# Optimization experiments

Hardware: AMD Instinct MI355X
Metric: run time of the kernel (lower is better)

The kernel has to match this reference:

```python
import jax, jax.numpy as jnp
import numpy as np

N, T, D_FEAT, D_GATE, D_MODEL = 1024, 32, 158, 63, 256
T_NHEAD, S_NHEAD, BETA = 4, 2, 5.0


def _pe(seq_len, d_model):
    pos = np.arange(seq_len, dtype=np.float32)[:, None]
    div = np.exp(np.arange(0, d_model, 2, dtype=np.float32) * (-np.log(10000.0) / d_model))
    pe = np.zeros((seq_len, d_model), np.float32)
    pe[:, 0::2] = np.sin(pos * div)
    pe[:, 1::2] = np.cos(pos * div)
    return jnp.asarray(pe)


def _ln(x, g, b):
    m = jnp.mean(x, -1, keepdims=True)
    v = jnp.var(x, -1, keepdims=True)
    return (x - m) / jnp.sqrt(v + 1e-5) * g + b


def _attn_block(x, n1g, n1b, Wq, Wk, Wv, n2g, n2b, W1, b1, W2, b2, nhead, over_stocks):
    # Faithful to SAttention/TAttention: per-head split of equally-sized dims is
    # equivalent to a single batched multi-head attention. Dropout p=0 (eval).
    n, t, d = x.shape
    dh = d // nhead
    temp = float(np.sqrt(d / nhead))
    xn = _ln(x, n1g, n1b)
    q = (xn @ Wq).reshape(n, t, nhead, dh)
    k = (xn @ Wk).reshape(n, t, nhead, dh)
    v = (xn @ Wv).reshape(n, t, nhead, dh)
    if over_stocks:
        # attention across stocks, per time step: scores [T,H,N,N]
        s = jnp.einsum('qthd,kthd->thqk', q, k) / temp
        a = jax.nn.softmax(s, -1)
        o = jnp.einsum('thqk,kthd->qthd', a, v).reshape(n, t, d)
    else:
        # attention across time, per stock: scores [N,H,T,T]
        s = jnp.einsum('nqhd,nkhd->nhqk', q, k) / temp
        a = jax.nn.softmax(s, -1)
        o = jnp.einsum('nhqk,nkhd->nqhd', a, v).reshape(n, t, d)
    xt = _ln(xn + o, n2g, n2b)
    ffn = jnp.maximum(xt @ W1 + b1, 0.0) @ W2 + b2
    return xt + ffn


def _forward(x, gate_W, gate_b, feat_W, feat_b, ds_mid_W, ds_mid_b, ds_small_W, ds_small_b,
             tn1g, tn1b, tWq, tWk, tWv, tn2g, tn2b, tW1, tb1, tW2, tb2,
             sn1g, sn1b, sWq, sWk, sWv, sn2g, sn2b, sW1, sb1, sW2, sb2,
             temp_W, fus_W, fus_b, fus_g, fus_bb, dec_W, dec_b):
    src = x[:, :, :D_FEAT]                       # [N,T,158]
    gate_in = x[:, -1, D_FEAT:]                  # [N,63] market features at last step
    g = D_FEAT * jax.nn.softmax((gate_in @ gate_W + gate_b) / BETA, -1)
    src = src * g[:, None, :]
    h = src @ feat_W + feat_b + _pe(T, D_MODEL)  # [N,32,256]
    # multi-scale downsampling: AvgPool1d k=2/s=2 and k=4/s=4 along time
    h_mid = h.reshape(N, T // 2, 2, D_MODEL).mean(2) @ ds_mid_W + ds_mid_b
    h_small = h.reshape(N, T // 4, 4, D_MODEL).mean(2) @ ds_small_W + ds_small_b
    pooled = []
    for hs in (h, h_mid, h_small):
        z = _attn_block(hs, tn1g, tn1b, tWq, tWk, tWv, tn2g, tn2b, tW1, tb1, tW2, tb2,
                        T_NHEAD, over_stocks=False)
        z = _attn_block(z, sn1g, sn1b, sWq, sWk, sWv, sn2g, sn2b, sW1, sb1, sW2, sb2,
                        S_NHEAD, over_stocks=True)
        # TemporalAttention pooling: query = last-step projection
        hh = z @ temp_W
        lam = jax.nn.softmax(jnp.einsum('ntd,nd->nt', hh, hh[:, -1, :]), -1)
        pooled.append(jnp.einsum('nt,ntd->nd', lam, z))
    fused = jnp.concatenate(pooled, -1) @ fus_W + fus_b
    fused = jnp.maximum(_ln(fused, fus_g, fus_bb), 0.0)
    return (fused @ dec_W + dec_b).squeeze(-1)    # [N]


def setup_inputs() -> dict:
    key = jax.random.key(0)
    ks = iter(jax.random.split(key, 40))
    w = lambda shape: jax.random.normal(next(ks), shape, jnp.float32) * 0.02
    d = D_MODEL
    inp = {
        'x': jax.random.normal(next(ks), (N, T, D_FEAT + D_GATE), jnp.float32),
        'gate_W': w((D_GATE, D_FEAT)), 'gate_b': jnp.zeros((D_FEAT,), jnp.float32),
        'feat_W': w((D_FEAT, d)), 'feat_b': jnp.zeros((d,), jnp.float32),
        'ds_mid_W': w((d, d)), 'ds_mid_b': jnp.zeros((d,), jnp.float32),
        'ds_small_W': w((d, d)), 'ds_small_b': jnp.zeros((d,), jnp.float32),
        'tn1g': jnp.ones((d,), jnp.float32), 'tn1b': jnp.zeros((d,), jnp.float32),
        'tWq': w((d, d)), 'tWk': w((d, d)), 'tWv': w((d, d)),
        'tn2g': jnp.ones((d,), jnp.float32), 'tn2b': jnp.zeros((d,), jnp.float32),
        'tW1': w((d, d)), 'tb1': jnp.zeros((d,), jnp.float32),
        'tW2': w((d, d)), 'tb2': jnp.zeros((d,), jnp.float32),
        'sn1g': jnp.ones((d,), jnp.float32), 'sn1b': jnp.zeros((d,), jnp.float32),
        'sWq': w((d, d)), 'sWk': w((d, d)), 'sWv': w((d, d)),
        'sn2g': jnp.ones((d,), jnp.float32), 'sn2b': jnp.zeros((d,), jnp.float32),
        'sW1': w((d, d)), 'sb1': jnp.zeros((d,), jnp.float32),
        'sW2': w((d, d)), 'sb2': jnp.zeros((d,), jnp.float32),
        'temp_W': w((d, d)),
        'fus_W': w((3 * d, d)), 'fus_b': jnp.zeros((d,), jnp.float32),
        'fus_g': jnp.ones((d,), jnp.float32), 'fus_bb': jnp.zeros((d,), jnp.float32),
        'dec_W': w((d, 1)), 'dec_b': jnp.zeros((1,), jnp.float32),
    }
    return inp


def reference(x, gate_W, gate_b, feat_W, feat_b, ds_mid_W, ds_mid_b, ds_small_W, ds_small_b,
              tn1g, tn1b, tWq, tWk, tWv, tn2g, tn2b, tW1, tb1, tW2, tb2,
              sn1g, sn1b, sWq, sWk, sWv, sn2g, sn2b, sW1, sb1, sW2, sb2,
              temp_W, fus_W, fus_b, fus_g, fus_bb, dec_W, dec_b):
    return _forward(x, gate_W, gate_b, feat_W, feat_b, ds_mid_W, ds_mid_b, ds_small_W, ds_small_b,
                    tn1g, tn1b, tWq, tWk, tWv, tn2g, tn2b, tW1, tb1, tW2, tb2,
                    sn1g, sn1b, sWq, sWk, sWv, sn2g, sn2b, sW1, sb1, sW2, sb2,
                    temp_W, fus_W, fus_b, fus_g, fus_bb, dec_W, dec_b)
```

## Files before the change

kernel.cpp:

```cpp
#include <hip/hip_runtime.h>
#include <math.h>

#define NS 1024
#define T0 32
#define DF 158
#define DG 63
#define DM 256
#define XROW (DF + DG)
#define MTOT 57344
#define B1R 32768
#define B2R 49152

typedef unsigned short u16;
typedef __attribute__((ext_vector_type(8))) short bf16x8_t;
typedef __attribute__((ext_vector_type(4))) float f32x4_t;

union frag_u {
  bf16x8_t f;
  unsigned short us[8];
  unsigned int u32[4];
};

__device__ inline unsigned short f2bf(float x) {
  unsigned int u = __float_as_uint(x);
  unsigned int r = u + 0x7fffu + ((u >> 16) & 1u);
  return (unsigned short)(r >> 16);
}
__device__ inline float bf2f(u16 u) {
  return __uint_as_float(((unsigned int)u) << 16);
}
__device__ inline unsigned int cvtpk(float a, float b) {
  unsigned int r;
  asm("v_cvt_pk_bf16_f32 %0, %1, %2" : "=v"(r) : "v"(a), "v"(b));
  return r;
}
__device__ inline void gl16(const u16* gp, unsigned char* lp) {
  __builtin_amdgcn_global_load_lds((const __attribute__((address_space(1))) unsigned int*)gp,
                                   (__attribute__((address_space(3))) unsigned int*)lp, 16, 0, 0);
}

__global__ void k_pe(float* __restrict__ pe) {
  int t = blockIdx.x, d = threadIdx.x;
  int i2 = d & ~1;
  float div = expf((float)i2 * (-logf(10000.0f) / (float)DM));
  float ang = (float)t * div;
  pe[t * DM + d] = (d & 1) ? cosf(ang) : sinf(ang);
}

__global__ void k_gate(const float* __restrict__ x, const float* __restrict__ gW,
                       const float* __restrict__ gb, float* __restrict__ g) {
  int n = blockIdx.x, tid = threadIdx.x;
  __shared__ float gin[DG];
  __shared__ float red[256];
  if (tid < DG) gin[tid] = x[(size_t)n * T0 * XROW + 31 * XROW + DF + tid];
  __syncthreads();
  float myv = 0.f;
  if (tid < DF) {
    float acc = gb[tid];
    for (int j = 0; j < DG; j++) acc = fmaf(gin[j], gW[j * DF + tid], acc);
    myv = acc * (1.0f / 5.0f);
  }
  red[tid] = (tid < DF) ? myv : -1e30f;
  __syncthreads();
  for (int s = 128; s > 0; s >>= 1) { if (tid < s) red[tid] = fmaxf(red[tid], red[tid + s]); __syncthreads(); }
  float mx = red[0];
  __syncthreads();
  float e = (tid < DF) ? expf(myv - mx) : 0.f;
  red[tid] = e;
  __syncthreads();
  for (int s = 128; s > 0; s >>= 1) { if (tid < s) red[tid] += red[tid + s]; __syncthreads(); }
  float sum = red[0];
  if (tid < DF) g[(size_t)n * DF + tid] = (float)DF * e / sum;
}

struct WPrep { const float* s[14]; float sc[14]; };
__global__ __launch_bounds__(256) void k_wprep(WPrep w, u16* __restrict__ dst) {
  int mat = blockIdx.x >> 4, nb = blockIdx.x & 15;
  int tid = threadIdx.x;
  int n = nb * 16 + (tid >> 4);
  int kc = (tid & 15) * 16;
  const float* src = w.s[mat];
  float sc = w.sc[mat];
  int K = (mat == 0) ? DF : 256;
  frag_u f0, f1;
#pragma unroll
  for (int j = 0; j < 8; j++) {
    int k0 = kc + j, k1 = kc + 8 + j;
    f0.us[j] = (k0 < K) ? f2bf(src[(size_t)k0 * 256 + n] * sc) : (u16)0;
    f1.us[j] = (k1 < K) ? f2bf(src[(size_t)k1 * 256 + n] * sc) : (u16)0;
  }
  u16* d = dst + (size_t)mat * 65536 + (size_t)n * 256 + kc;
  *(bf16x8_t*)d = f0.f;
  *(bf16x8_t*)(d + 8) = f1.f;
}

__global__ __launch_bounds__(256) void k_wtrans(const float* __restrict__ W, u16* __restrict__ Wt) {
  __shared__ u16 Ts[64][65];
  int k0 = blockIdx.x * 64, n0 = blockIdx.y * 64;
  int tid = threadIdx.x;
#pragma unroll
  for (int i = 0; i < 16; i++) {
    int e = tid + i * 256;
    int r = e >> 6, c = e & 63;
    Ts[r][c] = f2bf(W[(size_t)(k0 + r) * 256 + n0 + c]);
  }
  __syncthreads();
#pragma unroll
  for (int i = 0; i < 16; i++) {
    int e = tid + i * 256;
    int r = e >> 6, c = e & 63;
    Wt[(size_t)(n0 + r) * 768 + k0 + c] = Ts[c][r];
  }
}

template <bool BIAS, bool RELU, bool RES, bool OUTBF>
__global__ __launch_bounds__(256) void k_bgemm(
    const u16* __restrict__ A,
    const u16* __restrict__ B0, const u16* __restrict__ B1, const u16* __restrict__ B2,
    const float* __restrict__ bias, const u16* __restrict__ res,
    void* __restrict__ C0, void* __restrict__ C1, void* __restrict__ C2) {
  __shared__ __align__(16) unsigned char sm[32768];
  unsigned char* As = sm;
  unsigned char* Bs = sm + 16384;
  const u16* Bt = blockIdx.z == 0 ? B0 : (blockIdx.z == 1 ? B1 : B2);
  void* Cv = blockIdx.z == 0 ? C0 : (blockIdx.z == 1 ? C1 : C2);
  int m0 = blockIdx.y * 128, n0w = blockIdx.x * 128;
  int tid = threadIdx.x, lane = tid & 63, wid = tid >> 6;
  int qi = lane & 15, g = lane >> 4;
  int wr = wid >> 1, wc = wid & 1;
  f32x4_t acc[4][4];
#pragma unroll
  for (int i = 0; i < 4; i++)
#pragma unroll
    for (int j = 0; j < 4; j++) acc[i][j] = (f32x4_t){0.f, 0.f, 0.f, 0.f};
  for (int kt = 0; kt < 4; kt++) {
    if (kt) __syncthreads();
#pragma unroll
    for (int i = 0; i < 4; i++) {
      int cid = tid + i * 256;
      int row = cid >> 3, c = cid & 7;
      int cs = c ^ (row & 7);
      gl16(A + (size_t)(m0 + row) * 256 + kt * 64 + cs * 8, As + cid * 16);
      gl16(Bt + (size_t)(n0w + row) * 256 + kt * 64 + cs * 8, Bs + cid * 16);
    }
    __syncthreads();
    bf16x8_t Af[2][4], Bf[2][4];
#pragma unroll
    for (int mi = 0; mi < 4; mi++) {
      int row = wr * 64 + mi * 16 + qi;
      int swz = (row & 7) << 4;
      const unsigned char* ap = As + row * 128;
      Af[0][mi] = *(const bf16x8_t*)(ap + ((g * 16) ^ swz));
      Af[1][mi] = *(const bf16x8_t*)(ap + ((64 + g * 16) ^ swz));
    }
#pragma unroll
    for (int ni = 0; ni < 4; ni++) {
      int row = wc * 64 + ni * 16 + qi;
      int swz = (row & 7) << 4;
      const unsigned char* bp = Bs + row * 128;
      Bf[0][ni] = *(const bf16x8_t*)(bp + ((g * 16) ^ swz));
      Bf[1][ni] = *(const bf16x8_t*)(bp + ((64 + g * 16) ^ swz));
    }
#pragma unroll
    for (int ks = 0; ks < 2; ks++)
#pragma unroll
      for (int mi = 0; mi < 4; mi++)
#pragma unroll
        for (int ni = 0; ni < 4; ni++)
          acc[mi][ni] = __builtin_amdgcn_mfma_f32_16x16x32_bf16(Af[ks][mi], Bf[ks][ni], acc[mi][ni], 0, 0, 0);
  }
#pragma unroll
  for (int mi = 0; mi < 4; mi++) {
#pragma unroll
    for (int ni = 0; ni < 4; ni++) {
#pragma unroll
      for (int r = 0; r < 4; r++) {
        int row = m0 + wr * 64 + mi * 16 + 4 * g + r;
        int col = n0w + wc * 64 + ni * 16 + qi;
        float vv = acc[mi][ni][r];
        if (BIAS) vv += bias[col];
        if (RES) vv += bf2f(res[(size_t)row * 256 + col]);
        if (RELU) vv = fmaxf(vv, 0.f);
        if (OUTBF) ((u16*)Cv)[(size_t)row * 256 + col] = f2bf(vv);
        else ((float*)Cv)[(size_t)row * 256 + col] = vv;
      }
    }
  }
}

__global__ __launch_bounds__(256) void k_fgemm(
    const float* __restrict__ x, const float* __restrict__ gate,
    const u16* __restrict__ Bt, const float* __restrict__ bias,
    const float* __restrict__ pe, float* __restrict__ C) {
  __shared__ __align__(16) unsigned char sm[32768];
  unsigned char* As = sm;
  unsigned char* Bs = sm + 16384;
  int m0 = blockIdx.y * 128, n0w = blockIdx.x * 128;
  int tid = threadIdx.x, lane = tid & 63, wid = tid >> 6;
  int qi = lane & 15, g = lane >> 4;
  int wr = wid >> 1, wc = wid & 1;
  f32x4_t acc[4][4];
#pragma unroll
  for (int i = 0; i < 4; i++)
#pragma unroll
    for (int j = 0; j < 4; j++) acc[i][j] = (f32x4_t){0.f, 0.f, 0.f, 0.f};
  for (int kt = 0; kt < 3; kt++) {
    if (kt) __syncthreads();
#pragma unroll
    for (int i = 0; i < 4; i++) {
      int cid = tid + i * 256;
      int row = cid >> 3, c = cid & 7;
      int swz = (c * 16) ^ ((row & 7) << 4);
      int gk0 = kt * 64 + c * 8;
      const float* xr = x + (size_t)(m0 + row) * XROW;
      const float* gr = gate + (size_t)((m0 + row) >> 5) * DF;
      frag_u f;
#pragma unroll
      for (int j = 0; j < 8; j++) {
        int gk = gk0 + j;
        f.us[j] = (gk < DF) ? f2bf(xr[gk] * gr[gk]) : (u16)0;
      }
      *(bf16x8_t*)(As + row * 128 + swz) = f.f;
      bf16x8_t vb = *(const bf16x8_t*)(Bt + (size_t)(n0w + row) * 256 + kt * 64 + c * 8);
      *(bf16x8_t*)(Bs + row * 128 + swz) = vb;
    }
    __syncthreads();
    bf16x8_t Af[2][4], Bf[2][4];
#pragma unroll
    for (int mi = 0; mi < 4; mi++) {
      int row = wr * 64 + mi * 16 + qi;
      int swz = (row & 7) << 4;
      const unsigned char* ap = As + row * 128;
      Af[0][mi] = *(const bf16x8_t*)(ap + ((g * 16) ^ swz));
      Af[1][mi] = *(const bf16x8_t*)(ap + ((64 + g * 16) ^ swz));
    }
#pragma unroll
    for (int ni = 0; ni < 4; ni++) {
      int row = wc * 64 + ni * 16 + qi;
      int swz = (row & 7) << 4;
      const unsigned char* bp = Bs + row * 128;
      Bf[0][ni] = *(const bf16x8_t*)(bp + ((g * 16) ^ swz));
      Bf[1][ni] = *(const bf16x8_t*)(bp + ((64 + g * 16) ^ swz));
    }
#pragma unroll
    for (int ks = 0; ks < 2; ks++)
#pragma unroll
      for (int mi = 0; mi < 4; mi++)
#pragma unroll
        for (int ni = 0; ni < 4; ni++)
          acc[mi][ni] = __builtin_amdgcn_mfma_f32_16x16x32_bf16(Af[ks][mi], Bf[ks][ni], acc[mi][ni], 0, 0, 0);
  }
#pragma unroll
  for (int mi = 0; mi < 4; mi++) {
#pragma unroll
    for (int ni = 0; ni < 4; ni++) {
#pragma unroll
      for (int r = 0; r < 4; r++) {
        int row = m0 + wr * 64 + mi * 16 + 4 * g + r;
        int col = n0w + wc * 64 + ni * 16 + qi;
        C[(size_t)row * 256 + col] = acc[mi][ni][r] + bias[col] + pe[(row & (T0 - 1)) * DM + col];
      }
    }
  }
}

__global__ __launch_bounds__(256) void k_fus(const u16* __restrict__ A, const u16* __restrict__ Bt,
                                             const float* __restrict__ bias, float* __restrict__ C) {
  __shared__ __align__(16) unsigned char sm[16384];
  unsigned char* As = sm;
  unsigned char* Bs = sm + 8192;
  int n0 = blockIdx.x * 64, m0 = blockIdx.y * 64;
  int tid = threadIdx.x, lane = tid & 63, wid = tid >> 6;
  int qi = lane & 15, g = lane >> 4;
  f32x4_t acc[4];
#pragma unroll
  for (int i = 0; i < 4; i++) acc[i] = (f32x4_t){0.f, 0.f, 0.f, 0.f};
  for (int kt = 0; kt < 12; kt++) {
    if (kt) __syncthreads();
#pragma unroll
    for (int i = 0; i < 2; i++) {
      int cid = tid + i * 256;
      int row = cid >> 3, c = cid & 7;
      int swz = (c * 16) ^ ((row & 7) << 4);
      *(bf16x8_t*)(As + row * 128 + swz) = *(const bf16x8_t*)(A + (size_t)(m0 + row) * 768 + kt * 64 + c * 8);
      *(bf16x8_t*)(Bs + row * 128 + swz) = *(const bf16x8_t*)(Bt + (size_t)(n0 + row) * 768 + kt * 64 + c * 8);
    }
    __syncthreads();
    int arow = wid * 16 + qi;
    int asw = (arow & 7) << 4;
    bf16x8_t Af0 = *(const bf16x8_t*)(As + arow * 128 + ((g * 16) ^ asw));
    bf16x8_t Af1 = *(const bf16x8_t*)(As + arow * 128 + ((64 + g * 16) ^ asw));
#pragma unroll
    for (int ni = 0; ni < 4; ni++) {
      int brow = ni * 16 + qi;
      int bsw = (brow & 7) << 4;
      bf16x8_t B0 = *(const bf16x8_t*)(Bs + brow * 128 + ((g * 16) ^ bsw));
      bf16x8_t B1 = *(const bf16x8_t*)(Bs + brow * 128 + ((64 + g * 16) ^ bsw));
      acc[ni] = __builtin_amdgcn_mfma_f32_16x16x32_bf16(Af0, B0, acc[ni], 0, 0, 0);
      acc[ni] = __builtin_amdgcn_mfma_f32_16x16x32_bf16(Af1, B1, acc[ni], 0, 0, 0);
    }
  }
#pragma unroll
  for (int ni = 0; ni < 4; ni++)
#pragma unroll
    for (int r = 0; r < 4; r++) {
      int row = m0 + wid * 16 + 4 * g + r;
      int col = n0 + ni * 16 + qi;
      C[(size_t)row * 256 + col] = acc[ni][r] + bias[col];
    }
}

template <bool RES, bool ABF>
__global__ __launch_bounds__(256) void k_ln(const void* __restrict__ a, const float* __restrict__ b,
                                            const float* __restrict__ g, const float* __restrict__ be,
                                            u16* __restrict__ out) {
  int row = blockIdx.x * 4 + (threadIdx.x >> 6);
  int lane = threadIdx.x & 63;
  size_t base = (size_t)row * DM + lane * 4;
  float v[4];
  if (ABF) {
    ushort4 u = *(const ushort4*)((const u16*)a + base);
    v[0] = bf2f(u.x); v[1] = bf2f(u.y); v[2] = bf2f(u.z); v[3] = bf2f(u.w);
  } else {
    f32x4_t t = *(const f32x4_t*)((const float*)a + base);
    v[0] = t[0]; v[1] = t[1]; v[2] = t[2]; v[3] = t[3];
  }
  if (RES) {
    f32x4_t t = *(const f32x4_t*)(b + base);
    v[0] += t[0]; v[1] += t[1]; v[2] += t[2]; v[3] += t[3];
  }
  float s = v[0] + v[1] + v[2] + v[3];
#pragma unroll
  for (int off = 1; off < 64; off <<= 1) s += __shfl_xor(s, off);
  float mean = s * (1.0f / DM);
  float d0 = v[0] - mean, d1 = v[1] - mean, d2 = v[2] - mean, d3 = v[3] - mean;
  float ss = d0 * d0 + d1 * d1 + d2 * d2 + d3 * d3;
#pragma unroll
  for (int off = 1; off < 64; off <<= 1) ss += __shfl_xor(ss, off);
  float inv = rsqrtf(ss * (1.0f / DM) + 1e-5f);
  f32x4_t gg = *(const f32x4_t*)(g + lane * 4);
  f32x4_t bb = *(const f32x4_t*)(be + lane * 4);
  ushort4 o4;
  o4.x = f2bf(d0 * inv * gg[0] + bb[0]);
  o4.y = f2bf(d1 * inv * gg[1] + bb[1]);
  o4.z = f2bf(d2 * inv * gg[2] + bb[2]);
  o4.w = f2bf(d3 * inv * gg[3] + bb[3]);
  *(ushort4*)(out + base) = o4;
}

__global__ void k_poolmean(const float* __restrict__ h, u16* __restrict__ out, int Tout, int P) {
  int vi = blockIdx.x * 256 + threadIdx.x;
  int dv = vi & 63;
  int rowi = vi >> 6;
  int to = rowi % Tout;
  int n = rowi / Tout;
  int Tin = Tout * P;
  float s0 = 0.f, s1 = 0.f, s2 = 0.f, s3 = 0.f;
  for (int p = 0; p < P; p++) {
    f32x4_t t = *(const f32x4_t*)(h + ((size_t)(n * Tin + to * P + p)) * DM + dv * 4);
    s0 += t[0]; s1 += t[1]; s2 += t[2]; s3 += t[3];
  }
  float inv = 1.0f / (float)P;
  ushort4 o4;
  o4.x = f2bf(s0 * inv); o4.y = f2bf(s1 * inv); o4.z = f2bf(s2 * inv); o4.w = f2bf(s3 * inv);
  *(ushort4*)(out + (size_t)rowi * DM + dv * 4) = o4;
}

template <int T>
__global__ __launch_bounds__(256) void k_tattn(const u16* __restrict__ q, const u16* __restrict__ k,
                                               const u16* __restrict__ v, float* __restrict__ o) {
  constexpr int TR = (T < 16) ? 16 : T;
  constexpr int QKB = TR * 128;
  constexpr int HS = 2 * QKB + 64 * 80;
  __shared__ __align__(16) unsigned char smem[4 * HS];
  int n = blockIdx.x;
  int tid = threadIdx.x, lane = tid & 63, h = tid >> 6;
  int qi = lane & 15, g = lane >> 4;
  unsigned char* Qs = smem + h * HS;
  unsigned char* Ks = Qs + QKB;
  unsigned char* Vt = Ks + QKB;

  const u16* qh = q + (size_t)n * T * 256 + h * 64;
  const u16* kh = k + (size_t)n * T * 256 + h * 64;
  const u16* vh = v + (size_t)n * T * 256 + h * 64;
  const bf16x8_t zero8 = {0, 0, 0, 0, 0, 0, 0, 0};

  for (int idx = lane; idx < TR * 8; idx += 64) {
    int row = idx >> 3, c = idx & 7;
    bf16x8_t vq = zero8, vk = zero8;
    if (row < T) {
      vq = *(const bf16x8_t*)(qh + (size_t)row * 256 + c * 8);
      vk = *(const bf16x8_t*)(kh + (size_t)row * 256 + c * 8);
    }
    int off = row * 128 + ((c * 16) ^ ((row & 7) << 4));
    *(bf16x8_t*)(Qs + off) = vq;
    *(bf16x8_t*)(Ks + off) = vk;
  }
  {
    int kp = lane & 15, dg = lane >> 4;
    int d0 = dg * 16;
    int kk = 2 * kp;
    int cb = ((((kk >> 2) & 3) << 3) | (((kk >> 4) & 1) << 2) | (kk & 3)) * 2;
    frag_u a0, a1, b0, b1;
    a0.f = a1.f = b0.f = b1.f = zero8;
    if (kk < T) {
      a0.f = *(const bf16x8_t*)(vh + (size_t)kk * 256 + d0);
      a1.f = *(const bf16x8_t*)(vh + (size_t)kk * 256 + d0 + 8);
    }
    if (kk + 1 < T) {
      b0.f = *(const bf16x8_t*)(vh + (size_t)(kk + 1) * 256 + d0);
      b1.f = *(const bf16x8_t*)(vh + (size_t)(kk + 1) * 256 + d0 + 8);
    }
#pragma unroll
    for (int i = 0; i < 8; i++)
      *(unsigned int*)(Vt + (d0 + i) * 80 + cb) = (unsigned int)a0.us[i] | ((unsigned int)b0.us[i] << 16);
#pragma unroll
    for (int i = 0; i < 8; i++)
      *(unsigned int*)(Vt + (d0 + 8 + i) * 80 + cb) = (unsigned int)a1.us[i] | ((unsigned int)b1.us[i] << 16);
  }
  __syncthreads();

  constexpr int NQT = (T == 32) ? 2 : 1;
  constexpr int NSUB = (T == 32) ? 2 : 1;

  bf16x8_t Qb[NQT][2];
#pragma unroll
  for (int qt = 0; qt < NQT; qt++) {
    int row = qt * 16 + qi;
    int sw = (row & 7) << 4;
#pragma unroll
    for (int kst = 0; kst < 2; kst++)
      Qb[qt][kst] = *(const bf16x8_t*)(Qs + row * 128 + ((kst * 64 + g * 16) ^ sw));
  }
  f32x4_t sacc[NQT][NSUB];
#pragma unroll
  for (int qt = 0; qt < NQT; qt++)
#pragma unroll
    for (int sub = 0; sub < NSUB; sub++) sacc[qt][sub] = (f32x4_t){0.f, 0.f, 0.f, 0.f};
#pragma unroll
  for (int sub = 0; sub < NSUB; sub++) {
    int row = sub * 16 + qi;
    int sw = (row & 7) << 4;
    bf16x8_t Ka[2];
#pragma unroll
    for (int kst = 0; kst < 2; kst++)
      Ka[kst] = *(const bf16x8_t*)(Ks + row * 128 + ((kst * 64 + g * 16) ^ sw));
#pragma unroll
    for (int qt = 0; qt < NQT; qt++)
#pragma unroll
      for (int kst = 0; kst < 2; kst++)
        sacc[qt][sub] = __builtin_amdgcn_mfma_f32_16x16x32_bf16(Ka[kst], Qb[qt][kst], sacc[qt][sub], 0, 0, 0);
  }
  frag_u Pf[NQT];
#pragma unroll
  for (int qt = 0; qt < NQT; qt++) {
    float sv[NSUB][4];
    float mx = -3.0e38f;
#pragma unroll
    for (int sub = 0; sub < NSUB; sub++)
#pragma unroll
      for (int r = 0; r < 4; r++) {
        int key = sub * 16 + 4 * g + r;
        float s = sacc[qt][sub][r];
        if (key >= T) s = -3.0e38f;
        sv[sub][r] = s;
        mx = fmaxf(mx, s);
      }
    mx = fmaxf(mx, __shfl_xor(mx, 16));
    mx = fmaxf(mx, __shfl_xor(mx, 32));
    float p[NSUB][4];
    float l = 0.f;
#pragma unroll
    for (int sub = 0; sub < NSUB; sub++)
#pragma unroll
      for (int r = 0; r < 4; r++) {
        float e = exp2f(sv[sub][r] - mx);
        p[sub][r] = e;
        l += e;
      }
    l += __shfl_xor(l, 16);
    l += __shfl_xor(l, 32);
    float linv = 1.0f / l;
    Pf[qt].u32[0] = cvtpk(p[0][0] * linv, p[0][1] * linv);
    Pf[qt].u32[1] = cvtpk(p[0][2] * linv, p[0][3] * linv);
    if (NSUB == 2) {
      Pf[qt].u32[2] = cvtpk(p[NSUB - 1][0] * linv, p[NSUB - 1][1] * linv);
      Pf[qt].u32[3] = cvtpk(p[NSUB - 1][2] * linv, p[NSUB - 1][3] * linv);
    } else {
      Pf[qt].u32[2] = 0u;
      Pf[qt].u32[3] = 0u;
    }
  }
  f32x4_t oacc[NQT][4];
#pragma unroll
  for (int qt = 0; qt < NQT; qt++)
#pragma unroll
    for (int ni = 0; ni < 4; ni++) oacc[qt][ni] = (f32x4_t){0.f, 0.f, 0.f, 0.f};
#pragma unroll
  for (int ni = 0; ni < 4; ni++) {
    bf16x8_t Vb = *(const bf16x8_t*)(Vt + (ni * 16 + qi) * 80 + g * 16);
#pragma unroll
    for (int qt = 0; qt < NQT; qt++)
      oacc[qt][ni] = __builtin_amdgcn_mfma_f32_16x16x32_bf16(Pf[qt].f, Vb, oacc[qt][ni], 0, 0, 0);
  }
#pragma unroll
  for (int qt = 0; qt < NQT; qt++)
#pragma unroll
    for (int ni = 0; ni < 4; ni++)
#pragma unroll
      for (int r = 0; r < 4; r++) {
        int qq = qt * 16 + 4 * g + r;
        if (qq < T) o[((size_t)(n * T + qq)) * 256 + h * 64 + ni * 16 + qi] = oacc[qt][ni][r];
      }
}

__global__ __launch_bounds__(256) void k_sattn(const u16* __restrict__ q, const u16* __restrict__ k,
                                               const u16* __restrict__ v, float* __restrict__ o) {
  __shared__ __align__(16) unsigned char smem[32768];
  unsigned char* Ks = smem;
  unsigned char* Vt = smem + 16384;

  int bid = blockIdx.x;
  int T, rowbase;
  if (bid < 512) { T = 32; rowbase = 0; }
  else if (bid < 768) { T = 16; rowbase = B1R; bid -= 512; }
  else { T = 8; rowbase = B2R; bid -= 768; }
  const int NTH = T * 2;
  int xcd = bid & 7, slot = bid >> 3;
  int th = xcd * (NTH >> 3) + (slot >> 3);
  int qb = slot & 7;
  int t = th >> 1, h = th & 1;

  int tid = threadIdx.x;
  int lane = tid & 63;
  int wid = tid >> 6;
  int qi = lane & 15;
  int g = lane >> 4;

  const size_t rs = (size_t)T * 256;
  const size_t hb = (size_t)rowbase * 256 + (size_t)t * 256 + h * 128;
  const u16* qp = q + hb;
  const u16* kp = k + hb;
  const u16* vp = v + hb;
  float* op = o + hb;

  int q0 = qb * 128 + wid * 32;

  bf16x8_t QfA[4], QfB[4];
  {
    const u16* sA = qp + (size_t)(q0 + qi) * rs + g * 8;
    const u16* sB = sA + 16 * rs;
#pragma unroll
    for (int kst = 0; kst < 4; kst++) {
      QfA[kst] = *(const bf16x8_t*)(sA + kst * 32);
      QfB[kst] = *(const bf16x8_t*)(sB + kst * 32);
    }
  }

  f32x4_t OA[8], OB[8];
#pragma unroll
  for (int i = 0; i < 8; i++) {
    OA[i] = (f32x4_t){0.f, 0.f, 0.f, 0.f};
    OB[i] = (f32x4_t){0.f, 0.f, 0.f, 0.f};
  }
  float mA = -3.0e38f, lA = 0.f, mB = -3.0e38f, lB = 0.f;

  int kpair = tid & 31, dg = tid >> 5;
  int d0s = dg * 16;
  int kk = 2 * kpair;
  int cb = (((kk >> 5) << 5) | (((kk >> 2) & 3) << 3) | (((kk >> 4) & 1) << 2) | (kk & 3)) * 2;

  for (int kb = 0; kb < NS; kb += 64) {
    __syncthreads();
#pragma unroll
    for (int i = 0; i < 4; i++) {
      int cid = tid + i * 256;
      int row = cid >> 4, ch = cid & 15;
      bf16x8_t kv = *(const bf16x8_t*)(kp + (size_t)(kb + row) * rs + ch * 8);
      *(bf16x8_t*)(Ks + row * 256 + ((ch * 16) ^ ((row & 7) << 4))) = kv;
    }
    {
      const u16* s0 = vp + (size_t)(kb + kk) * rs + d0s;
      const u16* s1 = s0 + rs;
      frag_u a0, a1, b0, b1;
      a0.f = *(const bf16x8_t*)s0;
      a1.f = *(const bf16x8_t*)(s0 + 8);
      b0.f = *(const bf16x8_t*)s1;
      b1.f = *(const bf16x8_t*)(s1 + 8);
#pragma unroll
      for (int i = 0; i < 8; i++) {
        int d = d0s + i;
        *(unsigned int*)(Vt + d * 128 + (cb ^ ((d & 7) << 4))) =
            (unsigned int)a0.us[i] | ((unsigned int)b0.us[i] << 16);
      }
#pragma unroll
      for (int i = 0; i < 8; i++) {
        int d = d0s + 8 + i;
        *(unsigned int*)(Vt + d * 128 + (cb ^ ((d & 7) << 4))) =
            (unsigned int)a1.us[i] | ((unsigned int)b1.us[i] << 16);
      }
    }
    __syncthreads();

    f32x4_t saA[4], saB[4];
#pragma unroll
    for (int i = 0; i < 4; i++) {
      saA[i] = (f32x4_t){0.f, 0.f, 0.f, 0.f};
      saB[i] = (f32x4_t){0.f, 0.f, 0.f, 0.f};
    }
#pragma unroll
    for (int sub = 0; sub < 4; sub++) {
      int row = sub * 16 + qi;
      int swz = (row & 7) << 4;
      const unsigned char* kr = Ks + row * 256;
#pragma unroll
      for (int kst = 0; kst < 4; kst++) {
        bf16x8_t Af = *(const bf16x8_t*)(kr + ((g * 16 + kst * 64) ^ swz));
        saA[sub] = __builtin_amdgcn_mfma_f32_16x16x32_bf16(Af, QfA[kst], saA[sub], 0, 0, 0);
        saB[sub] = __builtin_amdgcn_mfma_f32_16x16x32_bf16(Af, QfB[kst], saB[sub], 0, 0, 0);
      }
    }

    float pmA = -3.0e38f, pmB = -3.0e38f;
#pragma unroll
    for (int sub = 0; sub < 4; sub++)
#pragma unroll
      for (int r = 0; r < 4; r++) {
        pmA = fmaxf(pmA, saA[sub][r]);
        pmB = fmaxf(pmB, saB[sub][r]);
      }
    pmA = fmaxf(pmA, __shfl_xor(pmA, 16));
    pmA = fmaxf(pmA, __shfl_xor(pmA, 32));
    pmB = fmaxf(pmB, __shfl_xor(pmB, 16));
    pmB = fmaxf(pmB, __shfl_xor(pmB, 32));
    if (__any(fmaxf(pmA - mA, pmB - mB) > 11.5f)) {
      float mnA = fmaxf(mA, pmA), mnB = fmaxf(mB, pmB);
      float fA = exp2f(mA - mnA), fB = exp2f(mB - mnB);
      lA *= fA;
      lB *= fB;
      float frA[4], frB[4];
#pragma unroll
      for (int r = 0; r < 4; r++) {
        frA[r] = __shfl(fA, (g << 2) | r);
        frB[r] = __shfl(fB, (g << 2) | r);
      }
#pragma unroll
      for (int dsub = 0; dsub < 8; dsub++)
#pragma unroll
        for (int r = 0; r < 4; r++) {
          OA[dsub][r] *= frA[r];
          OB[dsub][r] *= frB[r];
        }
      mA = mnA;
      mB = mnB;
    }
    float pA[4][4], pB[4][4];
    float lsA = 0.f, lsB = 0.f;
#pragma unroll
    for (int sub = 0; sub < 4; sub++)
#pragma unroll
      for (int r = 0; r < 4; r++) {
        float eA = exp2f(saA[sub][r] - mA);
        float eB = exp2f(saB[sub][r] - mB);
        pA[sub][r] = eA;
        pB[sub][r] = eB;
        lsA += eA;
        lsB += eB;
      }
    lsA += __shfl_xor(lsA, 16);
    lsA += __shfl_xor(lsA, 32);
    lsB += __shfl_xor(lsB, 16);
    lsB += __shfl_xor(lsB, 32);
    lA += lsA;
    lB += lsB;

    frag_u fA0, fA1, fB0, fB1;
    fA0.u32[0] = cvtpk(pA[0][0], pA[0][1]);
    fA0.u32[1] = cvtpk(pA[0][2], pA[0][3]);
    fA0.u32[2] = cvtpk(pA[1][0], pA[1][1]);
    fA0.u32[3] = cvtpk(pA[1][2], pA[1][3]);
    fA1.u32[0] = cvtpk(pA[2][0], pA[2][1]);
    fA1.u32[1] = cvtpk(pA[2][2], pA[2][3]);
    fA1.u32[2] = cvtpk(pA[3][0], pA[3][1]);
    fA1.u32[3] = cvtpk(pA[3][2], pA[3][3]);
    fB0.u32[0] = cvtpk(pB[0][0], pB[0][1]);
    fB0.u32[1] = cvtpk(pB[0][2], pB[0][3]);
    fB0.u32[2] = cvtpk(pB[1][0], pB[1][1]);
    fB0.u32[3] = cvtpk(pB[1][2], pB[1][3]);
    fB1.u32[0] = cvtpk(pB[2][0], pB[2][1]);
    fB1.u32[1] = cvtpk(pB[2][2], pB[2][3]);
    fB1.u32[2] = cvtpk(pB[3][0], pB[3][1]);
    fB1.u32[3] = cvtpk(pB[3][2], pB[3][3]);

#pragma unroll
    for (int kst = 0; kst < 2; kst++) {
      bf16x8_t PaA = kst ? fA1.f : fA0.f;
      bf16x8_t PaB = kst ? fB1.f : fB0.f;
#pragma unroll
      for (int dsub = 0; dsub < 8; dsub++) {
        int row = dsub * 16 + qi;
        bf16x8_t Vb = *(const bf16x8_t*)(Vt + row * 128 + ((g * 16 + kst * 64) ^ ((row & 7) << 4)));
        OA[dsub] = __builtin_amdgcn_mfma_f32_16x16x32_bf16(PaA, Vb, OA[dsub], 0, 0, 0);
        OB[dsub] = __builtin_amdgcn_mfma_f32_16x16x32_bf16(PaB, Vb, OB[dsub], 0, 0, 0);
      }
    }
  }

  float rinA[4], rinB[4];
#pragma unroll
  for (int r = 0; r < 4; r++) {
    rinA[r] = 1.0f / __shfl(lA, (g << 2) | r);
    rinB[r] = 1.0f / __shfl(lB, (g << 2) | r);
  }
#pragma unroll
  for (int dsub = 0; dsub < 8; dsub++)
#pragma unroll
    for (int r = 0; r < 4; r++) {
      size_t rowA = (size_t)(q0 + 4 * g + r);
      op[rowA * rs + dsub * 16 + qi] = OA[dsub][r] * rinA[r];
      op[(rowA + 16) * rs + dsub * 16 + qi] = OB[dsub][r] * rinB[r];
    }
}

__global__ __launch_bounds__(256) void k_tpool(const float* __restrict__ hh, const u16* __restrict__ z,
                                               u16* __restrict__ pooled, int T, int off) {
  int n = blockIdx.x;
  int tid = threadIdx.x, lane = tid & 63, w = tid >> 6;
  __shared__ float lam[T0];
  __shared__ float lame[T0];
  __shared__ float lsum;
  const float* hn = hh + (size_t)n * T * DM;
  f32x4_t last = *(const f32x4_t*)(hn + (size_t)(T - 1) * DM + lane * 4);
  for (int t = w; t < T; t += 4) {
    f32x4_t hv = *(const f32x4_t*)(hn + (size_t)t * DM + lane * 4);
    float s = hv[0] * last[0] + hv[1] * last[1] + hv[2] * last[2] + hv[3] * last[3];
#pragma unroll
    for (int o2 = 1; o2 < 64; o2 <<= 1) s += __shfl_xor(s, o2);
    if (lane == 0) lam[t] = s;
  }
  __syncthreads();
  if (tid < 64) {
    float vv = (lane < T) ? lam[lane] : -3.0e38f;
    float mx = vv;
#pragma unroll
    for (int o2 = 1; o2 < 64; o2 <<= 1) mx = fmaxf(mx, __shfl_xor(mx, o2));
    float e = (lane < T) ? expf(vv - mx) : 0.f;
    float su = e;
#pragma unroll
    for (int o2 = 1; o2 < 64; o2 <<= 1) su += __shfl_xor(su, o2);
    if (lane < T) lame[lane] = e;
    if (lane == 0) lsum = su;
  }
  __syncthreads();
  float acc = 0.f;
  const u16* zn = z + (size_t)n * T * DM + tid;
  for (int t = 0; t < T; t++) acc += lame[t] * bf2f(zn[(size_t)t * DM]);
  pooled[(size_t)n * 768 + off + tid] = f2bf(acc / lsum);
}

__global__ __launch_bounds__(256) void k_final(const float* __restrict__ f, const float* __restrict__ g,
                                               const float* __restrict__ b, const float* __restrict__ dw,
                                               const float* __restrict__ db, float* __restrict__ out) {
  int n = blockIdx.x, d = threadIdx.x;
  float v = f[(size_t)n * DM + d];
  __shared__ float red[256];
  red[d] = v;
  __syncthreads();
  for (int s = 128; s > 0; s >>= 1) { if (d < s) red[d] += red[d + s]; __syncthreads(); }
  float mean = red[0] * (1.0f / DM);
  __syncthreads();
  float dv = v - mean;
  red[d] = dv * dv;
  __syncthreads();
  for (int s = 128; s > 0; s >>= 1) { if (d < s) red[d] += red[d + s]; __syncthreads(); }
  float var = red[0] * (1.0f / DM);
  __syncthreads();
  float y = dv * rsqrtf(var + 1e-5f) * g[d] + b[d];
  y = fmaxf(y, 0.f);
  red[d] = y * dw[d];
  __syncthreads();
  for (int s = 128; s > 0; s >>= 1) { if (d < s) red[d] += red[d + s]; __syncthreads(); }
  if (d == 0) out[n] = red[0] + db[0];
}

extern "C" void kernel_launch(void* const* d_in, const int* in_sizes, int n_in,
                              void* d_out, int out_size, void* d_ws, size_t ws_size,
                              hipStream_t stream) {
  const float* x = (const float*)d_in[0];
  const float* gate_W = (const float*)d_in[1];
  const float* gate_b = (const float*)d_in[2];
  const float* feat_W = (const float*)d_in[3];
  const float* feat_b = (const float*)d_in[4];
  const float* ds_mid_W = (const float*)d_in[5];
  const float* ds_mid_b = (const float*)d_in[6];
  const float* ds_small_W = (const float*)d_in[7];
  const float* ds_small_b = (const float*)d_in[8];
  const float* tn1g = (const float*)d_in[9];
  const float* tn1b = (const float*)d_in[10];
  const float* tWq = (const float*)d_in[11];
  const float* tWk = (const float*)d_in[12];
  const float* tWv = (const float*)d_in[13];
  const float* tn2g = (const float*)d_in[14];
  const float* tn2b = (const float*)d_in[15];
  const float* tW1 = (const float*)d_in[16];
  const float* tb1 = (const float*)d_in[17];
  const float* tW2 = (const float*)d_in[18];
  const float* tb2 = (const float*)d_in[19];
  const float* sn1g = (const float*)d_in[20];
  const float* sn1b = (const float*)d_in[21];
  const float* sWq = (const float*)d_in[22];
  const float* sWk = (const float*)d_in[23];
  const float* sWv = (const float*)d_in[24];
  const float* sn2g = (const float*)d_in[25];
  const float* sn2b = (const float*)d_in[26];
  const float* sW1 = (const float*)d_in[27];
  const float* sb1 = (const float*)d_in[28];
  const float* sW2 = (const float*)d_in[29];
  const float* sb2 = (const float*)d_in[30];
  const float* temp_W = (const float*)d_in[31];
  const float* fus_W = (const float*)d_in[32];
  const float* fus_b = (const float*)d_in[33];
  const float* fus_g = (const float*)d_in[34];
  const float* fus_bb = (const float*)d_in[35];
  const float* dec_W = (const float*)d_in[36];
  const float* dec_b = (const float*)d_in[37];

  float* ws = (float*)d_ws;
  size_t o = 0;
  float* pe = ws + o; o += 8192;
  float* g = ws + o; o += 161792;
  u16* wt = (u16*)(ws + o); o += 458752;
  float* hcat = ws + o; o += (size_t)MTOT * 256;
  u16* bXNu = (u16*)(ws + o); o += (size_t)MTOT * 128;
  u16* bQu = (u16*)(ws + o); o += (size_t)MTOT * 128;
  u16* bKu = (u16*)(ws + o); o += (size_t)MTOT * 128;
  u16* bVu = (u16*)(ws + o); o += (size_t)MTOT * 128;
  float* bO = hcat;
  float* hh = hcat;
  float* fused = hcat;
  u16* pooledu = bXNu;
  u16* wFus = bKu;

  u16* wFeat = wt;
  u16* wDSm = wt + 1 * 65536;
  u16* wDSs = wt + 2 * 65536;
  u16* wTQ = wt + 3 * 65536;
  u16* wTK = wt + 4 * 65536;
  u16* wTV = wt + 5 * 65536;
  u16* wT1 = wt + 6 * 65536;
  u16* wT2 = wt + 7 * 65536;
  u16* wSQ = wt + 8 * 65536;
  u16* wSK = wt + 9 * 65536;
  u16* wSV = wt + 10 * 65536;
  u16* wS1 = wt + 11 * 65536;
  u16* wS2 = wt + 12 * 65536;
  u16* wTW = wt + 13 * 65536;

  k_pe<<<T0, DM, 0, stream>>>(pe);
  k_gate<<<NS, 256, 0, stream>>>(x, gate_W, gate_b, g);
  WPrep wp;
  wp.s[0] = feat_W; wp.s[1] = ds_mid_W; wp.s[2] = ds_small_W;
  wp.s[3] = tWq; wp.s[4] = tWk; wp.s[5] = tWv; wp.s[6] = tW1; wp.s[7] = tW2;
  wp.s[8] = sWq; wp.s[9] = sWk; wp.s[10] = sWv; wp.s[11] = sW1; wp.s[12] = sW2;
  wp.s[13] = temp_W;
  for (int i = 0; i < 14; i++) wp.sc[i] = 1.0f;
  wp.sc[3] = 0.125f * 1.4426950408889634f;
  wp.sc[8] = 0.08838834764831845f * 1.4426950408889634f;
  k_wprep<<<224, 256, 0, stream>>>(wp, wt);

  k_fgemm<<<dim3(2, 256), 256, 0, stream>>>(x, g, wFeat, feat_b, pe, hcat);
  k_poolmean<<<4096, 256, 0, stream>>>(hcat, bQu, 16, 2);
  k_bgemm<true, false, false, false><<<dim3(2, 128, 1), 256, 0, stream>>>(
      bQu, wDSm, wDSm, wDSm, ds_mid_b, nullptr, hcat + (size_t)B1R * 256, nullptr, nullptr);
  k_poolmean<<<2048, 256, 0, stream>>>(hcat, bQu, 8, 4);
  k_bgemm<true, false, false, false><<<dim3(2, 64, 1), 256, 0, stream>>>(
      bQu, wDSs, wDSs, wDSs, ds_small_b, nullptr, hcat + (size_t)B2R * 256, nullptr, nullptr);

  dim3 g1(2, MTOT / 128, 1), g3(2, MTOT / 128, 3);
  k_ln<false, false><<<MTOT / 4, 256, 0, stream>>>(hcat, nullptr, tn1g, tn1b, bXNu);
  k_bgemm<false, false, false, true><<<g3, 256, 0, stream>>>(
      bXNu, wTQ, wTK, wTV, nullptr, nullptr, bQu, bKu, bVu);
  k_tattn<32><<<NS, 256, 0, stream>>>(bQu, bKu, bVu, bO);
  k_tattn<16><<<NS, 256, 0, stream>>>(bQu + (size_t)B1R * 256, bKu + (size_t)B1R * 256,
                                      bVu + (size_t)B1R * 256, bO + (size_t)B1R * 256);
  k_tattn<8><<<NS, 256, 0, stream>>>(bQu + (size_t)B2R * 256, bKu + (size_t)B2R * 256,
                                     bVu + (size_t)B2R * 256, bO + (size_t)B2R * 256);
  k_ln<true, true><<<MTOT / 4, 256, 0, stream>>>(bXNu, bO, tn2g, tn2b, bQu);
  k_bgemm<true, true, false, true><<<g1, 256, 0, stream>>>(
      bQu, wT1, wT1, wT1, tb1, nullptr, bKu, nullptr, nullptr);
  k_bgemm<true, false, true, true><<<g1, 256, 0, stream>>>(
      bKu, wT2, wT2, wT2, tb2, bQu, bVu, nullptr, nullptr);
  k_ln<false, true><<<MTOT / 4, 256, 0, stream>>>(bVu, nullptr, sn1g, sn1b, bXNu);
  k_bgemm<false, false, false, true><<<g3, 256, 0, stream>>>(
      bXNu, wSQ, wSK, wSV, nullptr, nullptr, bQu, bKu, bVu);
  k_sattn<<<896, 256, 0, stream>>>(bQu, bKu, bVu, bO);
  k_ln<true, true><<<MTOT / 4, 256, 0, stream>>>(bXNu, bO, sn2g, sn2b, bQu);
  k_bgemm<true, true, false, true><<<g1, 256, 0, stream>>>(
      bQu, wS1, wS1, wS1, sb1, nullptr, bKu, nullptr, nullptr);
  k_bgemm<true, false, true, true><<<g1, 256, 0, stream>>>(
      bKu, wS2, wS2, wS2, sb2, bQu, bVu, nullptr, nullptr);
  k_bgemm<false, false, false, false><<<g1, 256, 0, stream>>>(
      bVu, wTW, wTW, wTW, nullptr, nullptr, hh, nullptr, nullptr);
  k_tpool<<<NS, 256, 0, stream>>>(hh, bVu, pooledu, 32, 0);
  k_tpool<<<NS, 256, 0, stream>>>(hh + (size_t)B1R * 256, bVu + (size_t)B1R * 256, pooledu, 16, 256);
  k_tpool<<<NS, 256, 0, stream>>>(hh + (size_t)B2R * 256, bVu + (size_t)B2R * 256, pooledu, 8, 512);

  k_wtrans<<<dim3(12, 4), 256, 0, stream>>>(fus_W, wFus);
  k_fus<<<dim3(4, 16), 256, 0, stream>>>(pooledu, wFus, fus_b, fused);
  k_final<<<NS, 256, 0, stream>>>(fused, fus_g, fus_bb, dec_W, dec_b, (float*)d_out);
}
```

Measured before the change: 497.7 us.

## Double-buffer LDS tiles in bf16 GEMM and stock-attention kernels

The bf16 GEMM and the cross-stock attention kernel now keep two shared-memory buffers, so the next K tile (and, for attention, the next K/V block) is fetched while MFMAs run on the current one. In attention, K is loaded directly into LDS with the async global-to-LDS path, and V is held in registers and written transposed after compute. This doubles LDS use to 64 KB per block, which may lower occupancy, and adds register pressure from the held V fragments.

```diff
diff --git a/kernel.cpp b/kernel.cpp
--- a/kernel.cpp
+++ b/kernel.cpp
@@ -119,9 +119,7 @@
     const u16* __restrict__ B0, const u16* __restrict__ B1, const u16* __restrict__ B2,
     const float* __restrict__ bias, const u16* __restrict__ res,
     void* __restrict__ C0, void* __restrict__ C1, void* __restrict__ C2) {
-  __shared__ __align__(16) unsigned char sm[32768];
-  unsigned char* As = sm;
-  unsigned char* Bs = sm + 16384;
+  __shared__ __align__(16) unsigned char sm[65536];
   const u16* Bt = blockIdx.z == 0 ? B0 : (blockIdx.z == 1 ? B1 : B2);
   void* Cv = blockIdx.z == 0 ? C0 : (blockIdx.z == 1 ? C1 : C2);
   int m0 = blockIdx.y * 128, n0w = blockIdx.x * 128;
@@ -133,17 +131,25 @@
   for (int i = 0; i < 4; i++)
 #pragma unroll
     for (int j = 0; j < 4; j++) acc[i][j] = (f32x4_t){0.f, 0.f, 0.f, 0.f};
-  for (int kt = 0; kt < 4; kt++) {
-    if (kt) __syncthreads();
+
+  auto stage = [&](int buf, int kt) {
 #pragma unroll
     for (int i = 0; i < 4; i++) {
       int cid = tid + i * 256;
       int row = cid >> 3, c = cid & 7;
       int cs = c ^ (row & 7);
-      gl16(A + (size_t)(m0 + row) * 256 + kt * 64 + cs * 8, As + cid * 16);
-      gl16(Bt + (size_t)(n0w + row) * 256 + kt * 64 + cs * 8, Bs + cid * 16);
-    }
-    __syncthreads();
+      gl16(A + (size_t)(m0 + row) * 256 + kt * 64 + cs * 8, sm + buf * 16384 + cid * 16);
+      gl16(Bt + (size_t)(n0w + row) * 256 + kt * 64 + cs * 8, sm + 32768 + buf * 16384 + cid * 16);
+    }
+  };
+
+  stage(0, 0);
+  __syncthreads();
+  int cur = 0;
+  for (int kt = 0; kt < 4; kt++) {
+    if (kt < 3) stage(cur ^ 1, kt + 1);
+    const unsigned char* As = sm + cur * 16384;
+    const unsigned char* Bs = sm + 32768 + cur * 16384;
     bf16x8_t Af[2][4], Bf[2][4];
 #pragma unroll
     for (int mi = 0; mi < 4; mi++) {
@@ -168,6 +174,8 @@
 #pragma unroll
         for (int ni = 0; ni < 4; ni++)
           acc[mi][ni] = __builtin_amdgcn_mfma_f32_16x16x32_bf16(Af[ks][mi], Bf[ks][ni], acc[mi][ni], 0, 0, 0);
+    __syncthreads();
+    cur ^= 1;
   }
 #pragma unroll
   for (int mi = 0; mi < 4; mi++) {
@@ -516,9 +524,7 @@
 
 __global__ __launch_bounds__(256) void k_sattn(const u16* __restrict__ q, const u16* __restrict__ k,
                                                const u16* __restrict__ v, float* __restrict__ o) {
-  __shared__ __align__(16) unsigned char smem[32768];
-  unsigned char* Ks = smem;
-  unsigned char* Vt = smem + 16384;
+  __shared__ __align__(16) unsigned char smem[65536];
 
   int bid = blockIdx.x;
   int T, rowbase;
@@ -570,37 +576,53 @@
   int kk = 2 * kpair;
   int cb = (((kk >> 5) << 5) | (((kk >> 2) & 3) << 3) | (((kk >> 4) & 1) << 2) | (kk & 3)) * 2;
 
-  for (int kb = 0; kb < NS; kb += 64) {
-    __syncthreads();
+  auto stageK = [&](int kb, int buf) {
+    unsigned char* kd = smem + buf * 16384;
 #pragma unroll
     for (int i = 0; i < 4; i++) {
       int cid = tid + i * 256;
-      int row = cid >> 4, ch = cid & 15;
-      bf16x8_t kv = *(const bf16x8_t*)(kp + (size_t)(kb + row) * rs + ch * 8);
-      *(bf16x8_t*)(Ks + row * 256 + ((ch * 16) ^ ((row & 7) << 4))) = kv;
-    }
-    {
-      const u16* s0 = vp + (size_t)(kb + kk) * rs + d0s;
-      const u16* s1 = s0 + rs;
-      frag_u a0, a1, b0, b1;
-      a0.f = *(const bf16x8_t*)s0;
-      a1.f = *(const bf16x8_t*)(s0 + 8);
-      b0.f = *(const bf16x8_t*)s1;
-      b1.f = *(const bf16x8_t*)(s1 + 8);
-#pragma unroll
-      for (int i = 0; i < 8; i++) {
-        int d = d0s + i;
-        *(unsigned int*)(Vt + d * 128 + (cb ^ ((d & 7) << 4))) =
-            (unsigned int)a0.us[i] | ((unsigned int)b0.us[i] << 16);
-      }
-#pragma unroll
-      for (int i = 0; i < 8; i++) {
-        int d = d0s + 8 + i;
-        *(unsigned int*)(Vt + d * 128 + (cb ^ ((d & 7) << 4))) =
-            (unsigned int)a1.us[i] | ((unsigned int)b1.us[i] << 16);
-      }
-    }
-    __syncthreads();
+      int row = cid >> 4, chp = cid & 15;
+      gl16(kp + (size_t)(kb + row) * rs + (size_t)((chp ^ (row & 7)) * 8), kd + cid * 16);
+    }
+  };
+  frag_u va0, va1, vb0, vb1;
+  auto loadV = [&](int kb) {
+    const u16* s0 = vp + (size_t)(kb + kk) * rs + d0s;
+    const u16* s1 = s0 + rs;
+    va0.f = *(const bf16x8_t*)s0;
+    va1.f = *(const bf16x8_t*)(s0 + 8);
+    vb0.f = *(const bf16x8_t*)s1;
+    vb1.f = *(const bf16x8_t*)(s1 + 8);
+  };
+  auto writeV = [&](int buf) {
+    unsigned char* Vt = smem + 32768 + buf * 16384;
+#pragma unroll
+    for (int i = 0; i < 8; i++) {
+      int d = d0s + i;
+      *(unsigned int*)(Vt + d * 128 + (cb ^ ((d & 7) << 4))) =
+          (unsigned int)va0.us[i] | ((unsigned int)vb0.us[i] << 16);
+    }
+#pragma unroll
+    for (int i = 0; i < 8; i++) {
+      int d = d0s + 8 + i;
+      *(unsigned int*)(Vt + d * 128 + (cb ^ ((d & 7) << 4))) =
+          (unsigned int)va1.us[i] | ((unsigned int)vb1.us[i] << 16);
+    }
+  };
+
+  stageK(0, 0);
+  loadV(0);
+  writeV(0);
+  __syncthreads();
+  int cur = 0;
+
+  for (int it = 0; it < 16; it++) {
+    if (it < 15) {
+      stageK((it + 1) * 64, cur ^ 1);
+      loadV((it + 1) * 64);
+    }
+    const unsigned char* Ks = smem + cur * 16384;
+    const unsigned char* Vt = smem + 32768 + cur * 16384;
 
     f32x4_t saA[4], saB[4];
 #pragma unroll
@@ -704,6 +726,10 @@
         OB[dsub] = __builtin_amdgcn_mfma_f32_16x16x32_bf16(PaB, Vb, OB[dsub], 0, 0, 0);
       }
     }
+
+    if (it < 15) writeV(cur ^ 1);
+    __syncthreads();
+    cur ^= 1;
   }
 
   float rinA[4], rinB[4];
```

New measurement: 587.3 us. +18.0%, slower.

## Read K fragments directly from global and double-buffer transposed V in LDS

Applied to the files above, without the earlier changes.

The stock-attention kernel no longer stages K tiles through shared memory. Each lane loads its K MFMA fragments straight from global memory. The freed LDS now holds a second V-transpose buffer, so the next V tile is prefetched into registers during compute and written to the alternate buffer, which leaves one barrier per iteration instead of two. The intent is to cut LDS traffic and synchronisation, at the risk of uncoalesced, cache-dependent global reads for K.

```diff
diff --git a/kernel.cpp b/kernel.cpp
--- a/kernel.cpp
+++ b/kernel.cpp
@@ -517,8 +517,6 @@
 __global__ __launch_bounds__(256) void k_sattn(const u16* __restrict__ q, const u16* __restrict__ k,
                                                const u16* __restrict__ v, float* __restrict__ o) {
   __shared__ __align__(16) unsigned char smem[32768];
-  unsigned char* Ks = smem;
-  unsigned char* Vt = smem + 16384;
 
   int bid = blockIdx.x;
   int T, rowbase;
@@ -570,37 +568,39 @@
   int kk = 2 * kpair;
   int cb = (((kk >> 5) << 5) | (((kk >> 2) & 3) << 3) | (((kk >> 4) & 1) << 2) | (kk & 3)) * 2;
 
-  for (int kb = 0; kb < NS; kb += 64) {
-    __syncthreads();
-#pragma unroll
-    for (int i = 0; i < 4; i++) {
-      int cid = tid + i * 256;
-      int row = cid >> 4, ch = cid & 15;
-      bf16x8_t kv = *(const bf16x8_t*)(kp + (size_t)(kb + row) * rs + ch * 8);
-      *(bf16x8_t*)(Ks + row * 256 + ((ch * 16) ^ ((row & 7) << 4))) = kv;
-    }
-    {
-      const u16* s0 = vp + (size_t)(kb + kk) * rs + d0s;
-      const u16* s1 = s0 + rs;
-      frag_u a0, a1, b0, b1;
-      a0.f = *(const bf16x8_t*)s0;
-      a1.f = *(const bf16x8_t*)(s0 + 8);
-      b0.f = *(const bf16x8_t*)s1;
-      b1.f = *(const bf16x8_t*)(s1 + 8);
-#pragma unroll
-      for (int i = 0; i < 8; i++) {
-        int d = d0s + i;
-        *(unsigned int*)(Vt + d * 128 + (cb ^ ((d & 7) << 4))) =
-            (unsigned int)a0.us[i] | ((unsigned int)b0.us[i] << 16);
-      }
-#pragma unroll
-      for (int i = 0; i < 8; i++) {
-        int d = d0s + 8 + i;
-        *(unsigned int*)(Vt + d * 128 + (cb ^ ((d & 7) << 4))) =
-            (unsigned int)a1.us[i] | ((unsigned int)b1.us[i] << 16);
-      }
-    }
-    __syncthreads();
+  frag_u va0, va1, vb0, vb1;
+  auto loadV = [&](int kb) {
+    const u16* s0 = vp + (size_t)(kb + kk) * rs + d0s;
+    const u16* s1 = s0 + rs;
+    va0.f = *(const bf16x8_t*)s0;
+    va1.f = *(const bf16x8_t*)(s0 + 8);
+    vb0.f = *(const bf16x8_t*)s1;
+    vb1.f = *(const bf16x8_t*)(s1 + 8);
+  };
+  auto writeV = [&](int buf) {
+    unsigned char* Vt = smem + buf * 16384;
+#pragma unroll
+    for (int i = 0; i < 8; i++) {
+      int d = d0s + i;
+      *(unsigned int*)(Vt + d * 128 + (cb ^ ((d & 7) << 4))) =
+          (unsigned int)va0.us[i] | ((unsigned int)vb0.us[i] << 16);
+    }
+#pragma unroll
+    for (int i = 0; i < 8; i++) {
+      int d = d0s + 8 + i;
+      *(unsigned int*)(Vt + d * 128 + (cb ^ ((d & 7) << 4))) =
+          (unsigned int)va1.us[i] | ((unsigned int)vb1.us[i] << 16);
+    }
+  };
+
+  loadV(0);
+  writeV(0);
+  __syncthreads();
+  int cur = 0;
+
+  for (int it = 0; it < 16; it++) {
+    int kb = it * 64;
+    if (it < 15) loadV(kb + 64);
 
     f32x4_t saA[4], saB[4];
 #pragma unroll
@@ -610,14 +610,14 @@
     }
 #pragma unroll
     for (int sub = 0; sub < 4; sub++) {
-      int row = sub * 16 + qi;
-      int swz = (row & 7) << 4;
-      const unsigned char* kr = Ks + row * 256;
+      const u16* kr = kp + (size_t)(kb + sub * 16 + qi) * rs + g * 8;
+      bf16x8_t Af[4];
+#pragma unroll
+      for (int kst = 0; kst < 4; kst++) Af[kst] = *(const bf16x8_t*)(kr + kst * 32);
 #pragma unroll
       for (int kst = 0; kst < 4; kst++) {
-        bf16x8_t Af = *(const bf16x8_t*)(kr + ((g * 16 + kst * 64) ^ swz));
-        saA[sub] = __builtin_amdgcn_mfma_f32_16x16x32_bf16(Af, QfA[kst], saA[sub], 0, 0, 0);
-        saB[sub] = __builtin_amdgcn_mfma_f32_16x16x32_bf16(Af, QfB[kst], saB[sub], 0, 0, 0);
+        saA[sub] = __builtin_amdgcn_mfma_f32_16x16x32_bf16(Af[kst], QfA[kst], saA[sub], 0, 0, 0);
+        saB[sub] = __builtin_amdgcn_mfma_f32_16x16x32_bf16(Af[kst], QfB[kst], saB[sub], 0, 0, 0);
       }
     }
 
@@ -692,6 +692,7 @@
     fB1.u32[2] = cvtpk(pB[3][0], pB[3][1]);
     fB1.u32[3] = cvtpk(pB[3][2], pB[3][3]);
 
+    const unsigned char* Vt = smem + cur * 16384;
 #pragma unroll
     for (int kst = 0; kst < 2; kst++) {
       bf16x8_t PaA = kst ? fA1.f : fA0.f;
@@ -704,6 +705,10 @@
         OB[dsub] = __builtin_amdgcn_mfma_f32_16x16x32_bf16(PaB, Vb, OB[dsub], 0, 0, 0);
       }
     }
+
+    if (it < 15) writeV(cur ^ 1);
+    __syncthreads();
+    cur ^= 1;
   }
 
   float rinA[4], rinB[4];
```

Result: slower. 677.3 us (+36.1%).
